# Kernel optimization log

Measured on AMD Instinct MI355X. Metric: run time of the kernel, lower is better.

## Reference

```python
import jax, jax.numpy as jnp
import numpy as np

TEMPERATURE = 0.1
THR = 0.2
BORDER_RM = 2


def setup_inputs() -> dict:
    key = jax.random.key(0)
    k0, k1 = jax.random.split(key)
    N, L, S, C = 2, 4800, 4800, 256
    return {
        "feat_c0": jax.random.normal(k0, (N, L, C), dtype=jnp.float32),
        "feat_c1": jax.random.normal(k1, (N, S, C), dtype=jnp.float32),
        "h0c": 60, "w0c": 80, "h1c": 60, "w1c": 80,
    }


def _border_valid(h, w, bd):
    # Faithful to torch mask_border: only the FIRST `bd` rows/cols are masked
    # (the negative slices m[:, -bd:0] in the source are empty no-ops).
    vh = jnp.arange(h) >= bd
    vw = jnp.arange(w) >= bd
    return (vh[:, None] & vw[None, :]).reshape(-1)  # [h*w]


def reference(feat_c0, feat_c1, h0c, w0c, h1c, w1c):
    C = feat_c0.shape[-1]
    scale = 1.0 / (C ** 0.5)  # 'sqrt_feat_dim' feature normalizer
    f0 = feat_c0 * scale
    f1 = feat_c1 * scale

    # dual-softmax confidence matrix [N, L, S]
    sim = jnp.einsum("nlc,nsc->nls", f0, f1) / TEMPERATURE
    conf = jax.nn.softmax(sim, axis=1) * jax.nn.softmax(sim, axis=2)

    # threshold + border removal (no padding masks in data)
    mask = conf > THR
    valid0 = _border_valid(h0c, w0c, BORDER_RM)  # [L]
    valid1 = _border_valid(h1c, w1c, BORDER_RM)  # [S]
    mask = mask & valid0[None, :, None] & valid1[None, None, :]

    # mutual nearest neighbour filtering
    mask = mask & (conf == conf.max(axis=2, keepdims=True)) \
                & (conf == conf.max(axis=1, keepdims=True))

    # match extraction (JIT-friendly padded form):
    # j_ids[b, i] = column of the (unique) True in row i; match_mask marks valid rows.
    j_ids = jnp.argmax(mask, axis=2)               # [N, L] int
    match_mask = jnp.any(mask, axis=2)             # [N, L] bool
    mconf = jnp.take_along_axis(conf, j_ids[..., None], axis=2)[..., 0]
    mconf = jnp.where(match_mask, mconf, 0.0)      # [N, L]

    return conf, match_mask, j_ids, mconf
```

## Files before the change

kernel.cpp:

```cpp
#include <hip/hip_runtime.h>


#define Ncst 2
#define Lc 4800
#define Sc 4800
#define Cc 256
#define K3 768
#define LP 4864
#define THRC 0.2f

typedef float f32x4 __attribute__((ext_vector_type(4)));
typedef __bf16 bf16x8 __attribute__((ext_vector_type(8)));

#define AS1(p) ((__attribute__((address_space(1))) void*)(p))
#define AS3(p) ((__attribute__((address_space(3))) void*)(p))

__device__ inline unsigned short f2bf(float x) {
    unsigned u = __float_as_uint(x);
    unsigned r = (u + 0x7fffu + ((u >> 16) & 1u)) >> 16;
    return (unsigned short)r;
}
__device__ inline float bf2f(unsigned short h) {
    return __uint_as_float(((unsigned)h) << 16);
}

__global__ __launch_bounds__(256) void init_kernel(float* __restrict__ rs, float* __restrict__ cs)
{
    int i = blockIdx.x * 256 + threadIdx.x;
    if (i < Ncst * Lc) { rs[i] = 0.f; cs[i] = 0.f; }
}

__global__ __launch_bounds__(256) void convert_kernel(
    const float* __restrict__ f0, const float* __restrict__ f1,
    unsigned short* __restrict__ A3, unsigned short* __restrict__ B3)
{
    int idx = blockIdx.x * 256 + threadIdx.x;
    if (idx >= Ncst * LP * (Cc / 8)) return;
    int k8  = idx & (Cc / 8 - 1);
    int row = (idx >> 5) % LP;
    int n   = idx / (LP * (Cc / 8));
    size_t base = ((size_t)n * LP + row) * K3 + k8 * 8;

    float av[8], bv[8];
    if (row < Lc) {
        const float4* pa = (const float4*)(f0 + ((size_t)n * Lc + row) * Cc + k8 * 8);
        float4 a0 = pa[0], a1 = pa[1];
        av[0]=a0.x; av[1]=a0.y; av[2]=a0.z; av[3]=a0.w;
        av[4]=a1.x; av[5]=a1.y; av[6]=a1.z; av[7]=a1.w;
        const float4* pb = (const float4*)(f1 + ((size_t)n * Sc + row) * Cc + k8 * 8);
        float4 b0 = pb[0], b1 = pb[1];
        bv[0]=b0.x; bv[1]=b0.y; bv[2]=b0.z; bv[3]=b0.w;
        bv[4]=b1.x; bv[5]=b1.y; bv[6]=b1.z; bv[7]=b1.w;
    } else {
        for (int i = 0; i < 8; ++i) { av[i] = 0.f; bv[i] = 0.f; }
    }

    unsigned short ahi[8], alo[8], bhi[8], blo[8];
#pragma unroll
    for (int i = 0; i < 8; ++i) {
        ahi[i] = f2bf(av[i]); alo[i] = f2bf(av[i] - bf2f(ahi[i]));
        bhi[i] = f2bf(bv[i]); blo[i] = f2bf(bv[i] - bf2f(bhi[i]));
    }
    *(uint4*)&A3[base]       = *(uint4*)ahi;
    *(uint4*)&A3[base + 256] = *(uint4*)ahi;
    *(uint4*)&A3[base + 512] = *(uint4*)alo;
    *(uint4*)&B3[base]       = *(uint4*)bhi;
    *(uint4*)&B3[base + 256] = *(uint4*)blo;
    *(uint4*)&B3[base + 512] = *(uint4*)bhi;
}

__global__ __launch_bounds__(256) void gemm_kernel(
    const unsigned short* __restrict__ A3, const unsigned short* __restrict__ B3,
    float* __restrict__ eout, float* __restrict__ rs, float* __restrict__ cs)
{
    __shared__ unsigned short lA[128 * 32];
    __shared__ unsigned short lB[128 * 32];

    const int n    = blockIdx.z;
    const int tm   = blockIdx.y;
    const int tn   = blockIdx.x;
    const int tid  = threadIdx.x;
    const int wave = tid >> 6;
    const int lane = tid & 63;
    const int wm   = wave >> 1;
    const int wn   = wave & 1;
    const int ml   = lane & 15;
    const int kq   = lane >> 4;

    const unsigned short* Ab = A3 + ((size_t)n * LP + (size_t)tm * 128) * K3;
    const unsigned short* Bb = B3 + ((size_t)n * LP + (size_t)tn * 128) * K3;

    f32x4 acc[4][4] = {};

    for (int k0 = 0; k0 < K3; k0 += 32) {
        __syncthreads();
#pragma unroll
        for (int cc = 0; cc < 2; ++cc) {
            int c    = wave * 2 + cc;
            int slot = c * 64 + lane;
            int row  = slot >> 2;
            int q    = (slot & 3) ^ ((row >> 1) & 3);
            const unsigned short* ga = Ab + (size_t)row * K3 + (k0 + q * 8);
            const unsigned short* gb = Bb + (size_t)row * K3 + (k0 + q * 8);
            __builtin_amdgcn_global_load_lds(AS1(ga), AS3(lA + (size_t)slot * 8), 16, 0, 0);
            __builtin_amdgcn_global_load_lds(AS1(gb), AS3(lB + (size_t)slot * 8), 16, 0, 0);
        }
        __syncthreads();

        bf16x8 af[4], bfr[4];
#pragma unroll
        for (int i = 0; i < 4; ++i) {
            int arow = wm * 64 + i * 16 + ml;
            int aslot = arow * 4 + (kq ^ ((arow >> 1) & 3));
            af[i] = *(const bf16x8*)&lA[aslot * 8];
            int brow = wn * 64 + i * 16 + ml;
            int bslot = brow * 4 + (kq ^ ((brow >> 1) & 3));
            bfr[i] = *(const bf16x8*)&lB[bslot * 8];
        }
#pragma unroll
        for (int i = 0; i < 4; ++i)
#pragma unroll
            for (int j = 0; j < 4; ++j)
                acc[i][j] = __builtin_amdgcn_mfma_f32_16x16x32_bf16(af[i], bfr[j], acc[i][j], 0, 0, 0);
    }

    const float alpha = 5.0f / 128.0f;
#pragma unroll
    for (int i = 0; i < 4; ++i) {
#pragma unroll
        for (int r = 0; r < 4; ++r) {
            int gl = tm * 128 + wm * 64 + i * 16 + kq * 4 + r;
            bool rok = gl < Lc;
#pragma unroll
            for (int j = 0; j < 4; ++j) {
                int gs = tn * 128 + wn * 64 + j * 16 + ml;
                bool ok = rok && (gs < Sc);
                float ev = ok ? __expf(acc[i][j][r] * alpha) : 0.f;
                acc[i][j][r] = ev;
                if (ok) eout[((size_t)n * Lc + gl) * Sc + gs] = ev;
            }
        }
    }
#pragma unroll
    for (int i = 0; i < 4; ++i) {
#pragma unroll
        for (int r = 0; r < 4; ++r) {
            float rp = acc[i][0][r] + acc[i][1][r] + acc[i][2][r] + acc[i][3][r];
            rp += __shfl_xor(rp, 1);
            rp += __shfl_xor(rp, 2);
            rp += __shfl_xor(rp, 4);
            rp += __shfl_xor(rp, 8);
            int gl = tm * 128 + wm * 64 + i * 16 + kq * 4 + r;
            if (ml == 0 && gl < Lc) atomicAdd(&rs[(size_t)n * Lc + gl], rp);
        }
    }
#pragma unroll
    for (int j = 0; j < 4; ++j) {
        float cp = 0.f;
#pragma unroll
        for (int i = 0; i < 4; ++i)
#pragma unroll
            for (int r = 0; r < 4; ++r) cp += acc[i][j][r];
        cp += __shfl_xor(cp, 16);
        cp += __shfl_xor(cp, 32);
        int gs = tn * 128 + wn * 64 + j * 16 + ml;
        if (kq == 0 && gs < Sc) atomicAdd(&cs[(size_t)n * Sc + gs], cp);
    }
}

__global__ __launch_bounds__(256) void inv_kernel(
    const float* __restrict__ rs, const float* __restrict__ cs,
    float* __restrict__ rsinv, float* __restrict__ csinv)
{
    int i = blockIdx.x * 256 + threadIdx.x;
    if (i < Ncst * Lc) { rsinv[i] = 1.0f / rs[i]; csinv[i] = 1.0f / cs[i]; }
}

__global__ __launch_bounds__(256) void conf_kernel(
    float* __restrict__ confio,
    const float* __restrict__ rsinv, const float* __restrict__ csinv,
    float* __restrict__ rcm)
{
    __shared__ float sh[256];
    int b = blockIdx.x;
    int n = b / Lc;
    f32x4* row = (f32x4*)(confio + (size_t)b * Sc);
    const f32x4* civ = (const f32x4*)(csinv + (size_t)n * Sc);
    int tid = threadIdx.x;
    float riv = rsinv[b];
    float lmax = 0.f;
    for (int v = tid; v < Sc / 4; v += 256) {
        f32x4 e4 = row[v];
        f32x4 c4 = civ[v];
        f32x4 o  = e4 * e4 * riv * c4;
        row[v] = o;
        lmax = fmaxf(lmax, fmaxf(fmaxf(o.x, o.y), fmaxf(o.z, o.w)));
    }
    sh[tid] = lmax;
    __syncthreads();
    for (int off = 128; off; off >>= 1) {
        if (tid < off) sh[tid] = fmaxf(sh[tid], sh[tid + off]);
        __syncthreads();
    }
    if (tid == 0) rcm[b] = sh[0];
}

__global__ __launch_bounds__(256) void finalize_kernel(
    const float* __restrict__ conf, const float* __restrict__ rcm,
    const int* __restrict__ h0p, const int* __restrict__ w0p,
    const int* __restrict__ h1p, const int* __restrict__ w1p,
    float* __restrict__ out_match, float* __restrict__ out_j, float* __restrict__ out_mconf)
{
    int i = blockIdx.x * 256 + threadIdx.x;
    if (i >= Ncst * Lc) return;
    int n = i / Lc, l = i % Lc;
    float mm = rcm[i];
    float fm = 0.f, fj = 0.f, fc = 0.f;
    if (mm > THRC) {
        int w0 = *w0p, w1 = *w1p;
        if ((l / w0) >= 2 && (l % w0) >= 2) {
            const float* rowp = conf + ((size_t)n * Lc + l) * Sc;
            for (int s = 0; s < Sc; ++s) {
                float c = rowp[s];
                if (c == mm && (s / w1) >= 2 && (s % w1) >= 2) {
                    bool ismax = true;
                    const float* colp = conf + (size_t)n * Lc * Sc + s;
                    for (int lp = 0; lp < Lc; ++lp) {
                        if (colp[(size_t)lp * Sc] > c) { ismax = false; break; }
                    }
                    if (ismax) { fm = 1.f; fj = (float)s; fc = c; break; }
                }
            }
        }
    }
    out_match[i] = fm; out_j[i] = fj; out_mconf[i] = fc;
}

extern "C" void kernel_launch(void* const* d_in, const int* in_sizes, int n_in,
                              void* d_out, int out_size, void* d_ws, size_t ws_size,
                              hipStream_t stream) {
    const float* f0 = (const float*)d_in[0];
    const float* f1 = (const float*)d_in[1];
    const int* h0p = (const int*)d_in[2];
    const int* w0p = (const int*)d_in[3];
    const int* h1p = (const int*)d_in[4];
    const int* w1p = (const int*)d_in[5];

    char* ws = (char*)d_ws;
    unsigned short* A3 = (unsigned short*)ws;
    unsigned short* B3 = (unsigned short*)(ws + 14942208);
    float* rs    = (float*)(ws + 29884416);
    float* cs    = (float*)(ws + 29922816);
    float* rsinv = (float*)(ws + 29961216);
    float* csinv = (float*)(ws + 29999616);
    float* rcm   = (float*)(ws + 30038016);

    float* conf      = (float*)d_out;
    float* out_match = conf + (size_t)Ncst * Lc * Sc;
    float* out_j     = out_match + Ncst * Lc;
    float* out_mconf = out_j + Ncst * Lc;

    init_kernel<<<(Ncst * Lc + 255) / 256, 256, 0, stream>>>(rs, cs);

    convert_kernel<<<(Ncst * LP * (Cc / 8) + 255) / 256, 256, 0, stream>>>(f0, f1, A3, B3);

    dim3 gg(LP / 128, LP / 128, Ncst);
    gemm_kernel<<<gg, 256, 0, stream>>>(A3, B3, conf, rs, cs);

    inv_kernel<<<(Ncst * Lc + 255) / 256, 256, 0, stream>>>(rs, cs, rsinv, csinv);

    conf_kernel<<<Ncst * Lc, 256, 0, stream>>>(conf, rsinv, csinv, rcm);

    finalize_kernel<<<(Ncst * Lc + 255) / 256, 256, 0, stream>>>(
        conf, rcm, h0p, w0p, h1p, w1p, out_match, out_j, out_mconf);
}
```

Baseline: 359.5 us.

## Fuse init/inv kernels, widen GEMM K-tile, block-reduce sums, wave-per-row conf

Folds the zero-init into the convert kernel and drops the reciprocal kernel, computing rcp inline in the conf pass. The GEMM K-step doubles to 64 with a new 8-way XOR swizzle, and row/col partial sums are combined in LDS before one atomic per row/column per block. The conf kernel now maps one wave per row with shuffle max reduction and nontemporal stores. This trades fewer launches, syncs and atomics for more LDS per GEMM block and per-element reciprocal work.

```diff
diff --git a/kernel.cpp b/kernel.cpp
--- a/kernel.cpp
+++ b/kernel.cpp
@@ -24,17 +24,13 @@
     return __uint_as_float(((unsigned)h) << 16);
 }
 
-__global__ __launch_bounds__(256) void init_kernel(float* __restrict__ rs, float* __restrict__ cs)
-{
-    int i = blockIdx.x * 256 + threadIdx.x;
-    if (i < Ncst * Lc) { rs[i] = 0.f; cs[i] = 0.f; }
-}
-
 __global__ __launch_bounds__(256) void convert_kernel(
     const float* __restrict__ f0, const float* __restrict__ f1,
-    unsigned short* __restrict__ A3, unsigned short* __restrict__ B3)
+    unsigned short* __restrict__ A3, unsigned short* __restrict__ B3,
+    float* __restrict__ rs, float* __restrict__ cs)
 {
     int idx = blockIdx.x * 256 + threadIdx.x;
+    if (idx < Ncst * Lc) { rs[idx] = 0.f; cs[idx] = 0.f; }
     if (idx >= Ncst * LP * (Cc / 8)) return;
     int k8  = idx & (Cc / 8 - 1);
     int row = (idx >> 5) % LP;
@@ -73,8 +69,8 @@
     const unsigned short* __restrict__ A3, const unsigned short* __restrict__ B3,
     float* __restrict__ eout, float* __restrict__ rs, float* __restrict__ cs)
 {
-    __shared__ unsigned short lA[128 * 32];
-    __shared__ unsigned short lB[128 * 32];
+    __shared__ unsigned short lA[128 * 64];
+    __shared__ unsigned short lB[128 * 64];
 
     const int n    = blockIdx.z;
     const int tm   = blockIdx.y;
@@ -92,37 +88,41 @@
 
     f32x4 acc[4][4] = {};
 
-    for (int k0 = 0; k0 < K3; k0 += 32) {
+    for (int k0 = 0; k0 < K3; k0 += 64) {
         __syncthreads();
 #pragma unroll
-        for (int cc = 0; cc < 2; ++cc) {
-            int c    = wave * 2 + cc;
+        for (int cc = 0; cc < 4; ++cc) {
+            int c    = wave * 4 + cc;
             int slot = c * 64 + lane;
-            int row  = slot >> 2;
-            int q    = (slot & 3) ^ ((row >> 1) & 3);
-            const unsigned short* ga = Ab + (size_t)row * K3 + (k0 + q * 8);
-            const unsigned short* gb = Bb + (size_t)row * K3 + (k0 + q * 8);
+            int row  = slot >> 3;
+            int ql   = (slot & 7) ^ (row & 7);
+            const unsigned short* ga = Ab + (size_t)row * K3 + (k0 + ql * 8);
+            const unsigned short* gb = Bb + (size_t)row * K3 + (k0 + ql * 8);
             __builtin_amdgcn_global_load_lds(AS1(ga), AS3(lA + (size_t)slot * 8), 16, 0, 0);
             __builtin_amdgcn_global_load_lds(AS1(gb), AS3(lB + (size_t)slot * 8), 16, 0, 0);
         }
         __syncthreads();
 
-        bf16x8 af[4], bfr[4];
-#pragma unroll
-        for (int i = 0; i < 4; ++i) {
-            int arow = wm * 64 + i * 16 + ml;
-            int aslot = arow * 4 + (kq ^ ((arow >> 1) & 3));
-            af[i] = *(const bf16x8*)&lA[aslot * 8];
-            int brow = wn * 64 + i * 16 + ml;
-            int bslot = brow * 4 + (kq ^ ((brow >> 1) & 3));
-            bfr[i] = *(const bf16x8*)&lB[bslot * 8];
-        }
-#pragma unroll
-        for (int i = 0; i < 4; ++i)
-#pragma unroll
-            for (int j = 0; j < 4; ++j)
-                acc[i][j] = __builtin_amdgcn_mfma_f32_16x16x32_bf16(af[i], bfr[j], acc[i][j], 0, 0, 0);
-    }
+#pragma unroll
+        for (int half = 0; half < 2; ++half) {
+            bf16x8 af[4], bfr[4];
+#pragma unroll
+            for (int i = 0; i < 4; ++i) {
+                int arow  = wm * 64 + i * 16 + ml;
+                int aslot = arow * 8 + ((half * 4 + kq) ^ (arow & 7));
+                af[i] = *(const bf16x8*)&lA[(size_t)aslot * 8];
+                int brow  = wn * 64 + i * 16 + ml;
+                int bslot = brow * 8 + ((half * 4 + kq) ^ (brow & 7));
+                bfr[i] = *(const bf16x8*)&lB[(size_t)bslot * 8];
+            }
+#pragma unroll
+            for (int i = 0; i < 4; ++i)
+#pragma unroll
+                for (int j = 0; j < 4; ++j)
+                    acc[i][j] = __builtin_amdgcn_mfma_f32_16x16x32_bf16(af[i], bfr[j], acc[i][j], 0, 0, 0);
+        }
+    }
+    __syncthreads();
 
     const float alpha = 5.0f / 128.0f;
 #pragma unroll
@@ -141,6 +141,8 @@
             }
         }
     }
+
+    float* red = (float*)lA;
 #pragma unroll
     for (int i = 0; i < 4; ++i) {
 #pragma unroll
@@ -150,8 +152,7 @@
             rp += __shfl_xor(rp, 2);
             rp += __shfl_xor(rp, 4);
             rp += __shfl_xor(rp, 8);
-            int gl = tm * 128 + wm * 64 + i * 16 + kq * 4 + r;
-            if (ml == 0 && gl < Lc) atomicAdd(&rs[(size_t)n * Lc + gl], rp);
+            if (ml == 0) red[wn * 128 + wm * 64 + i * 16 + kq * 4 + r] = rp;
         }
     }
 #pragma unroll
@@ -163,46 +164,50 @@
             for (int r = 0; r < 4; ++r) cp += acc[i][j][r];
         cp += __shfl_xor(cp, 16);
         cp += __shfl_xor(cp, 32);
-        int gs = tn * 128 + wn * 64 + j * 16 + ml;
-        if (kq == 0 && gs < Sc) atomicAdd(&cs[(size_t)n * Sc + gs], cp);
-    }
-}
-
-__global__ __launch_bounds__(256) void inv_kernel(
-    const float* __restrict__ rs, const float* __restrict__ cs,
-    float* __restrict__ rsinv, float* __restrict__ csinv)
-{
-    int i = blockIdx.x * 256 + threadIdx.x;
-    if (i < Ncst * Lc) { rsinv[i] = 1.0f / rs[i]; csinv[i] = 1.0f / cs[i]; }
+        if (kq == 0) red[256 + wm * 128 + wn * 64 + j * 16 + ml] = cp;
+    }
+    __syncthreads();
+    if (tid < 128) {
+        int gl = tm * 128 + tid;
+        if (gl < Lc) atomicAdd(&rs[(size_t)n * Lc + gl], red[tid] + red[128 + tid]);
+    } else {
+        int t = tid - 128;
+        int gs = tn * 128 + t;
+        if (gs < Sc) atomicAdd(&cs[(size_t)n * Sc + gs], red[256 + t] + red[384 + t]);
+    }
 }
 
 __global__ __launch_bounds__(256) void conf_kernel(
     float* __restrict__ confio,
-    const float* __restrict__ rsinv, const float* __restrict__ csinv,
+    const float* __restrict__ rs, const float* __restrict__ cs,
     float* __restrict__ rcm)
 {
-    __shared__ float sh[256];
-    int b = blockIdx.x;
-    int n = b / Lc;
+    const int wave = threadIdx.x >> 6;
+    const int lane = threadIdx.x & 63;
+    const int b = blockIdx.x * 4 + wave;
+    const int n = b / Lc;
     f32x4* row = (f32x4*)(confio + (size_t)b * Sc);
-    const f32x4* civ = (const f32x4*)(csinv + (size_t)n * Sc);
-    int tid = threadIdx.x;
-    float riv = rsinv[b];
+    const f32x4* csv = (const f32x4*)(cs + (size_t)n * Sc);
+    const float riv = __builtin_amdgcn_rcpf(rs[b]);
     float lmax = 0.f;
-    for (int v = tid; v < Sc / 4; v += 256) {
-        f32x4 e4 = row[v];
-        f32x4 c4 = civ[v];
-        f32x4 o  = e4 * e4 * riv * c4;
-        row[v] = o;
+    for (int g = lane; g < Sc / 4; g += 64) {
+        f32x4 e4 = row[g];
+        f32x4 c4 = csv[g];
+        f32x4 o;
+        o.x = e4.x * e4.x * riv * __builtin_amdgcn_rcpf(c4.x);
+        o.y = e4.y * e4.y * riv * __builtin_amdgcn_rcpf(c4.y);
+        o.z = e4.z * e4.z * riv * __builtin_amdgcn_rcpf(c4.z);
+        o.w = e4.w * e4.w * riv * __builtin_amdgcn_rcpf(c4.w);
+        __builtin_nontemporal_store(o, &row[g]);
         lmax = fmaxf(lmax, fmaxf(fmaxf(o.x, o.y), fmaxf(o.z, o.w)));
     }
-    sh[tid] = lmax;
-    __syncthreads();
-    for (int off = 128; off; off >>= 1) {
-        if (tid < off) sh[tid] = fmaxf(sh[tid], sh[tid + off]);
-        __syncthreads();
-    }
-    if (tid == 0) rcm[b] = sh[0];
+    lmax = fmaxf(lmax, __shfl_xor(lmax, 1));
+    lmax = fmaxf(lmax, __shfl_xor(lmax, 2));
+    lmax = fmaxf(lmax, __shfl_xor(lmax, 4));
+    lmax = fmaxf(lmax, __shfl_xor(lmax, 8));
+    lmax = fmaxf(lmax, __shfl_xor(lmax, 16));
+    lmax = fmaxf(lmax, __shfl_xor(lmax, 32));
+    if (lane == 0) rcm[b] = lmax;
 }
 
 __global__ __launch_bounds__(256) void finalize_kernel(
@@ -249,27 +254,21 @@
     char* ws = (char*)d_ws;
     unsigned short* A3 = (unsigned short*)ws;
     unsigned short* B3 = (unsigned short*)(ws + 14942208);
-    float* rs    = (float*)(ws + 29884416);
-    float* cs    = (float*)(ws + 29922816);
-    float* rsinv = (float*)(ws + 29961216);
-    float* csinv = (float*)(ws + 29999616);
-    float* rcm   = (float*)(ws + 30038016);
+    float* rs  = (float*)(ws + 29884416);
+    float* cs  = (float*)(ws + 29922816);
+    float* rcm = (float*)(ws + 29961216);
 
     float* conf      = (float*)d_out;
     float* out_match = conf + (size_t)Ncst * Lc * Sc;
     float* out_j     = out_match + Ncst * Lc;
     float* out_mconf = out_j + Ncst * Lc;
 
-    init_kernel<<<(Ncst * Lc + 255) / 256, 256, 0, stream>>>(rs, cs);
-
-    convert_kernel<<<(Ncst * LP * (Cc / 8) + 255) / 256, 256, 0, stream>>>(f0, f1, A3, B3);
+    convert_kernel<<<(Ncst * LP * (Cc / 8) + 255) / 256, 256, 0, stream>>>(f0, f1, A3, B3, rs, cs);
 
     dim3 gg(LP / 128, LP / 128, Ncst);
     gemm_kernel<<<gg, 256, 0, stream>>>(A3, B3, conf, rs, cs);
 
-    inv_kernel<<<(Ncst * Lc + 255) / 256, 256, 0, stream>>>(rs, cs, rsinv, csinv);
-
-    conf_kernel<<<Ncst * Lc, 256, 0, stream>>>(conf, rsinv, csinv, rcm);
+    conf_kernel<<<Ncst * Lc / 4, 256, 0, stream>>>(conf, rs, cs, rcm);
 
     finalize_kernel<<<(Ncst * Lc + 255) / 256, 256, 0, stream>>>(
         conf, rcm, h0p, w0p, h1p, w1p, out_match, out_j, out_mconf);
```

Measured after the change: 363.3 us. No clear change (+1.1%).
